# Performance work log

Measured on AMD Instinct MI355X. Metric: run time of the kernel, lower is better.

The kernel has to match this reference:

```python
import jax, jax.numpy as jnp
import numpy as np

D_MODEL, D_INNER, D_CONV, D_STATE, DT_RANK = 1024, 2048, 4, 16, 64
ALPHA, CHUNK = 0.1, 64


def setup_inputs() -> dict:
    key = jax.random.key(0)
    ks = jax.random.split(key, 10)
    B, T = 2, 2048
    s = lambda k, shape, scale: jax.random.normal(k, shape, jnp.float32) * scale
    return {
        "x": s(ks[0], (B, T, D_MODEL), 1.0),
        "norm1_w": jnp.ones((D_MODEL,), jnp.float32),
        "norm2_w": jnp.ones((D_MODEL,), jnp.float32),
        "in_proj_w": s(ks[1], (2 * D_INNER, D_MODEL), 0.02),
        "in_proj_b": jnp.zeros((2 * D_INNER,), jnp.float32),
        "conv_w": s(ks[2], (D_INNER, 1, D_CONV), 0.1),
        "conv_b": jnp.zeros((D_INNER,), jnp.float32),
        "x_proj_w": s(ks[3], (DT_RANK + 2 * D_STATE, D_INNER), 0.02),
        "dt_proj_w": s(ks[4], (D_INNER, DT_RANK), 0.02),
        "dt_proj_b": s(ks[5], (D_INNER,), 0.02),
        "A_log": jnp.log(jnp.broadcast_to(jnp.arange(1, D_STATE + 1, dtype=jnp.float32), (D_INNER, D_STATE))) + 0.0,
        "D_ssm": jnp.ones((D_INNER,), jnp.float32),
        "out_proj_w": s(ks[6], (D_MODEL, D_INNER), 0.02),
        "out_proj_b": jnp.zeros((D_MODEL,), jnp.float32),
        "proj_write_w": s(ks[7], (D_MODEL, D_MODEL), 0.02),
        "proj_read_w": s(ks[8], (D_MODEL, D_MODEL), 0.02),
        "decay": jnp.float32(4.6),
    }


def rmsnorm(x, w, eps=1e-5):
    return x * jax.lax.rsqrt(jnp.mean(x * x, axis=-1, keepdims=True) + eps) * w


def mamba_block(x, in_w, in_b, conv_w, conv_b, xp_w, dt_w, dt_b, A_log, D_ssm, out_w, out_b):
    # canonical (mamba-minimal) selective-SSM block
    B, T, _ = x.shape
    xz = x @ in_w.T + in_b                      # (B,T,2*d_inner)
    xm, res = jnp.split(xz, 2, axis=-1)
    # causal depthwise conv over time
    xc = jax.lax.conv_general_dilated(
        xm.transpose(0, 2, 1), conv_w, (1,), [(D_CONV - 1, 0)],
        dimension_numbers=("NCH", "OIH", "NCH"), feature_group_count=D_INNER)
    xm = jax.nn.silu(xc.transpose(0, 2, 1) + conv_b)
    x_dbl = xm @ xp_w.T                         # (B,T,dt_rank+2*d_state)
    delta = jax.nn.softplus(x_dbl[..., :DT_RANK] @ dt_w.T + dt_b)
    Bm = x_dbl[..., DT_RANK:DT_RANK + D_STATE]
    Cm = x_dbl[..., DT_RANK + D_STATE:]
    A = -jnp.exp(A_log)                          # (d_inner, d_state)

    def step(h, ins):
        d_t, B_t, C_t, u_t = ins                 # (B,di),(B,ds),(B,ds),(B,di)
        dA = jnp.exp(d_t[:, :, None] * A)
        h = h * dA + (d_t * u_t)[:, :, None] * B_t[:, None, :]
        y = jnp.einsum("bds,bs->bd", h, C_t)
        return h, y

    h0 = jnp.zeros((B, D_INNER, D_STATE), x.dtype)
    _, ys = jax.lax.scan(step, h0, (delta.transpose(1, 0, 2), Bm.transpose(1, 0, 2),
                                    Cm.transpose(1, 0, 2), xm.transpose(1, 0, 2)))
    y = ys.transpose(1, 0, 2) + xm * D_ssm
    y = y * jax.nn.silu(res)
    return y @ out_w.T + out_b


def memory_attend(out, w_write, w_read, decay):
    # chunked Hebbian write/read (RetNet-style chunked linear attention)
    B, T, D = out.shape
    C = CHUNK
    gamma = jax.nn.sigmoid(decay)
    log_gamma = jnp.log(gamma)
    v = out @ w_write.T
    wk = jnp.pad(out[:, :-1], ((0, 0), (1, 0), (0, 0)))
    rk = out
    n = T // C
    p = jnp.arange(C)
    diffs = jnp.clip(p[:, None] - 1 - p[None, :], 0, None).astype(out.dtype)
    causal = (p[:, None] > p[None, :]).astype(out.dtype)
    M = jnp.exp(diffs * log_gamma) * causal      # (C,C) intra-chunk decay mask
    g_in = gamma ** p                            # (C,)
    g_w = gamma ** (C - 1 - p)                   # (C,)

    chunked = lambda a: a.reshape(B, n, C, D).transpose(1, 0, 2, 3)  # (n,B,C,D)

    def step(W, ins):
        rk_c, wk_c, v_c = ins                    # each (B,C,D)
        inter = jnp.einsum("bde,bce->bcd", W, rk_c) * g_in[None, :, None]
        S = jnp.einsum("bcd,bkd->bck", rk_c, wk_c)
        intra = jnp.einsum("bck,bkd->bcd", S * M, v_c)
        W_new = (gamma ** C) * W + jnp.einsum("bcd,bce->bde", v_c * g_w[None, :, None], wk_c)
        return W_new, inter + intra

    W0 = jnp.zeros((B, D, D), out.dtype)
    _, reads = jax.lax.scan(step, W0, (chunked(rk), chunked(wk), chunked(v)))
    reads = reads.transpose(1, 0, 2, 3).reshape(B, T, D)
    return out + ALPHA * (reads @ w_read.T)


def reference(x, norm1_w, norm2_w, in_proj_w, in_proj_b, conv_w, conv_b, x_proj_w,
              dt_proj_w, dt_proj_b, A_log, D_ssm, out_proj_w, out_proj_b,
              proj_write_w, proj_read_w, decay):
    mb = lambda h: mamba_block(h, in_proj_w, in_proj_b, conv_w, conv_b, x_proj_w,
                               dt_proj_w, dt_proj_b, A_log, D_ssm, out_proj_w, out_proj_b)
    out1 = mb(rmsnorm(x, norm1_w))
    x1 = x + out1
    out2 = mb(rmsnorm(x1, norm2_w))   # tied weights: same params as mamba1
    out2 = memory_attend(out2, proj_write_w, proj_read_w, decay)
    return x1 + out2
```

## Files before the change

### kernel.cpp

```cpp
#include <hip/hip_runtime.h>
#include <hip/hip_bf16.h>
#include <math.h>

typedef __hip_bfloat16 bf16;
typedef __attribute__((ext_vector_type(4))) float f32x4;
typedef __attribute__((ext_vector_type(8))) short bf16x8;
typedef __attribute__((ext_vector_type(8))) unsigned short u16x8;

static __device__ __forceinline__ float b2f(bf16 v) { return __bfloat162float(v); }
static __device__ __forceinline__ float us2f(unsigned short u) {
  union { unsigned short s; bf16 h; } c; c.s = u; return __bfloat162float(c.h);
}
static __device__ __forceinline__ void  stv(float* p, float v) { *p = v; }
static __device__ __forceinline__ void  stv(bf16* p, float v) { *p = __float2bfloat16(v); }
static __device__ __forceinline__ float ldin(const void* p, size_t i, int f) {
  return f ? ((const float*)p)[i] : b2f(((const bf16*)p)[i]);
}
static __device__ __forceinline__ unsigned short f2b(float x) {
  bf16 h = __float2bfloat16(x);
  return *reinterpret_cast<unsigned short*>(&h);
}

static __device__ __forceinline__ void gl16(const unsigned short* g,
                                            void* ldsbase, int byteoff) {
  __builtin_amdgcn_global_load_lds(
      (const __attribute__((address_space(1))) unsigned int*)g,
      (__attribute__((address_space(3))) unsigned int*)((char*)ldsbase + byteoff),
      16, 0, 0);
}

constexpr int B_  = 2;
constexpr int T_  = 2048;
constexpr int DM  = 1024;
constexpr int DI  = 2048;
constexpr int DS  = 16;
constexpr int DTR = 64;
constexpr int ROWS = B_ * T_;
constexpr int SL  = 32;
constexpr int NSC = T_ / SL;
constexpr int KSP = 4;

__global__ void detect_k(const void* __restrict__ decay, int* __restrict__ flag) {
  flag[0] = (((const unsigned short*)decay)[0] == 0x4093) ? 0 : 1;
  flag[1] = 0;
}

__global__ void sentinel_k(void* __restrict__ out, float val, int n,
                           const int* __restrict__ df) {
  int f = *df;
  int i = blockIdx.x * 256 + threadIdx.x;
  if (i < n) {
    if (f) ((float*)out)[i] = val;
    else   ((bf16*)out)[i] = __float2bfloat16(val);
  }
}

__global__ void cvt1_k(const void* __restrict__ src, bf16* __restrict__ dst, int n,
                       const int* __restrict__ df) {
  int f = *df;
  int i = blockIdx.x * 256 + threadIdx.x;
  if (i < n) stv(&dst[i], ldin(src, i, f));
}

__global__ void rmsnorm_k(const void* __restrict__ xin, const void* __restrict__ w,
                          bf16* __restrict__ out, const int* __restrict__ df,
                          int xin_raw) {
  int f = *df;
  int fx = xin_raw ? f : 0;
  int row = blockIdx.x;
  int tid = threadIdx.x;
  float ss = 0.f;
  for (int d = tid; d < DM; d += 256) {
    float v = ldin(xin, (size_t)row * DM + d, fx);
    ss += v * v;
  }
  for (int o = 32; o > 0; o >>= 1) ss += __shfl_down(ss, o, 64);
  __shared__ float sred[4];
  int lane = tid & 63, wid = tid >> 6;
  if (lane == 0) sred[wid] = ss;
  __syncthreads();
  if (tid == 0) {
    float t = sred[0] + sred[1] + sred[2] + sred[3];
    sred[0] = 1.f / sqrtf(t / DM + 1e-5f);
  }
  __syncthreads();
  float rs = sred[0];
  for (int d = tid; d < DM; d += 256) {
    float v = ldin(xin, (size_t)row * DM + d, fx);
    stv(&out[(size_t)row * DM + d], v * rs * ldin(w, d, f));
  }
}

__global__ void transpose_k(const bf16* __restrict__ src, bf16* __restrict__ dst) {
  __shared__ unsigned short tile[64][65];
  int b = blockIdx.z;
  int t0 = blockIdx.x * 64, d0 = blockIdx.y * 64;
  int tid = threadIdx.x;
  int lt = tid & 63, lq = tid >> 6;
  const unsigned short* sp = (const unsigned short*)src;
  unsigned short* dp = (unsigned short*)dst;
#pragma unroll
  for (int i = 0; i < 16; i++) {
    int r = lq * 16 + i;
    tile[r][lt] = sp[((size_t)b * T_ + t0 + r) * DM + d0 + lt];
  }
  __syncthreads();
#pragma unroll
  for (int i = 0; i < 16; i++) {
    int r = lq * 16 + i;
    dp[((size_t)b * DM + d0 + r) * T_ + t0 + lt] = tile[lt][r];
  }
}

template <int MODE, int ACT, int MROWS>
__global__ void mgemm_k(const bf16* __restrict__ A, size_t sAz, int lda,
                        const void* __restrict__ B, size_t sBz, int ldb,
                        const void* __restrict__ bias,
                        bf16* __restrict__ C, size_t sCz, int ldc,
                        int M, int N, int K,
                        const void* __restrict__ dec, const int* __restrict__ df) {
  constexpr int FR = MROWS / 32;
  int by = (MODE == 2) ? ((int)gridDim.y - 1 - (int)blockIdx.y) : (int)blockIdx.y;
  int m0 = by * MROWS, n0 = blockIdx.x * 128;
  if (MODE == 1 && n0 > m0 + MROWS - 1) return;
  int f = *df;
  int bz = blockIdx.z;
  const bf16* Ab = A + (size_t)bz * sAz;
  const unsigned short* Bb16 =
      (const unsigned short*)B + (size_t)bz * sBz;
  bf16* Cb = C + (size_t)bz * sCz;
  int kmax = (MODE == 2) ? (m0 + MROWS) : K;
  __shared__ alignas(16) unsigned short As[2][MROWS][32];
  __shared__ alignas(16) unsigned short Bs[2][128][32];
  int tid = threadIdx.x;
  int wave = tid >> 6, lane = tid & 63, quad = lane >> 4, l15 = lane & 15;
  int wr = (wave >> 1) * (MROWS / 2), wc = (wave & 1) * 64;
  f32x4 acc[FR][4] = {};
  int lrow = lane >> 2;
  int lh   = (lane & 3) * 8;
  const unsigned short* Aus = (const unsigned short*)Ab;

  auto stage = [&](int buf, int k0) {
    if (MROWS == 128) {
#pragma unroll
      for (int q = 0; q < 2; q++) {
        int seg = wave * 2 + q;
        int rowa = seg * 16 + lrow;
        gl16(Aus + (size_t)(m0 + rowa) * lda + k0 + lh, &As[buf][0][0],
             seg * 1024);
      }
    } else {
      int rowa = wave * 16 + lrow;
      gl16(Aus + (size_t)(m0 + rowa) * lda + k0 + lh, &As[buf][0][0],
           wave * 1024);
    }
    if (MODE == 0 && f) {
      int r = tid >> 1, h = (tid & 1) * 16;
      const float* bp = (const float*)B + (size_t)(n0 + r) * ldb + k0 + h;
      float4 x0 = *(const float4*)bp,       x1 = *(const float4*)(bp + 4);
      float4 x2 = *(const float4*)(bp + 8), x3 = *(const float4*)(bp + 12);
      union { unsigned short s[8]; uint4 v; } p0, p1;
      p0.s[0]=f2b(x0.x); p0.s[1]=f2b(x0.y); p0.s[2]=f2b(x0.z); p0.s[3]=f2b(x0.w);
      p0.s[4]=f2b(x1.x); p0.s[5]=f2b(x1.y); p0.s[6]=f2b(x1.z); p0.s[7]=f2b(x1.w);
      p1.s[0]=f2b(x2.x); p1.s[1]=f2b(x2.y); p1.s[2]=f2b(x2.z); p1.s[3]=f2b(x2.w);
      p1.s[4]=f2b(x3.x); p1.s[5]=f2b(x3.y); p1.s[6]=f2b(x3.z); p1.s[7]=f2b(x3.w);
      *(uint4*)&Bs[buf][r][h]     = p0.v;
      *(uint4*)&Bs[buf][r][h + 8] = p1.v;
    } else {
#pragma unroll
      for (int q = 0; q < 2; q++) {
        int seg = wave * 2 + q;
        int rowb = seg * 16 + lrow;
        gl16(Bb16 + (size_t)(n0 + rowb) * ldb + k0 + lh, &Bs[buf][0][0],
             seg * 1024);
      }
    }
  };

  auto compute = [&](int buf) {
    bf16x8 af[FR], bfv[4];
#pragma unroll
    for (int i = 0; i < FR; i++)
      af[i] = *(const bf16x8*)&As[buf][wr + 16 * i + l15][quad * 8];
#pragma unroll
    for (int j = 0; j < 4; j++)
      bfv[j] = *(const bf16x8*)&Bs[buf][wc + 16 * j + l15][quad * 8];
#pragma unroll
    for (int i = 0; i < FR; i++)
#pragma unroll
      for (int j = 0; j < 4; j++)
        acc[i][j] = __builtin_amdgcn_mfma_f32_16x16x32_bf16(af[i], bfv[j],
                                                            acc[i][j], 0, 0, 0);
  };

  int nt = kmax >> 5;
  stage(0, 0);
  __syncthreads();
  int cur = 0;
  for (int t = 0; t < nt - 1; ++t) {
    stage(cur ^ 1, (t + 1) * 32);
    compute(cur);
    __syncthreads();
    cur ^= 1;
  }
  compute(cur);

  float lg = 0.f;
  if (MODE == 1) {
    float g = 1.f / (1.f + __expf(-ldin(dec, 0, f)));
    lg = __logf(g);
  }
#pragma unroll
  for (int i = 0; i < FR; i++) {
#pragma unroll
    for (int rr = 0; rr < 4; rr++) {
      int row = m0 + wr + 16 * i + quad * 4 + rr;
      if (MODE == 1 && n0 == 0 && wc == 0 && l15 == 0)
        Cb[(size_t)row * ldc] = __float2bfloat16(0.f);
#pragma unroll
      for (int j = 0; j < 4; j++) {
        int col = n0 + wc + 16 * j + l15;
        float v = acc[i][j][rr];
        if (MODE == 0) {
          if (bias) v += ldin(bias, col, f);
          if (ACT == 1) v = (v > 20.f) ? v : log1pf(__expf(v));
          Cb[(size_t)row * ldc + col] = __float2bfloat16(v);
        } else if (MODE == 1) {
          int colp = col + 1;
          int d_ = row - colp;
          v = (d_ > 0) ? v * __expf(lg * (float)(d_ - 1)) : 0.f;
          if (colp < N)
            Cb[(size_t)row * ldc + colp] = __float2bfloat16(v);
        } else {
          Cb[(size_t)row * ldc + col] = __float2bfloat16(v);
        }
      }
    }
  }
}

__global__ void conv_silu_k(const bf16* __restrict__ xz, const void* __restrict__ cw,
                            const void* __restrict__ cb, bf16* __restrict__ xm,
                            const int* __restrict__ df) {
  int f = *df;
  int i = blockIdx.x * 256 + threadIdx.x;
  int d = i & (DI - 1);
  int t = (i >> 11) & (T_ - 1);
  int b = i >> 22;
  const bf16* base = xz + (size_t)b * T_ * 2 * DI + d;
  float s = ldin(cb, d, f);
#pragma unroll
  for (int k = 0; k < 4; k++) {
    int tt = t - 3 + k;
    if (tt >= 0) s += ldin(cw, d * 4 + k, f) * b2f(base[(size_t)tt * 2 * DI]);
  }
  stv(&xm[i], s / (1.f + __expf(-s)));
}

__global__ void xproj_k(const bf16* __restrict__ xm, const void* __restrict__ xpw,
                        bf16* __restrict__ parts, const int* __restrict__ df) {
  int f = *df;
  int m0 = blockIdx.x * 128;
  int z = blockIdx.y;
  int kbase = z * (DI / KSP);
  __shared__ alignas(16) unsigned short As[2][128][32];
  __shared__ alignas(16) unsigned short Bs[2][96][32];
  int tid = threadIdx.x;
  int wave = tid >> 6, lane = tid & 63, quad = lane >> 4, l15 = lane & 15;
  int wr = wave * 32;
  f32x4 acc[2][6] = {};
  int lrow = lane >> 2;
  int lh   = (lane & 3) * 8;
  const unsigned short* Aus = (const unsigned short*)xm;
  const unsigned short* Bus = (const unsigned short*)xpw;

  auto stage = [&](int buf, int k0) {
#pragma unroll
    for (int q = 0; q < 2; q++) {
      int seg = wave * 2 + q;
      int rowa = seg * 16 + lrow;
      gl16(Aus + (size_t)(m0 + rowa) * DI + kbase + k0 + lh, &As[buf][0][0],
           seg * 1024);
    }
    if (f) {
      if (tid < 192) {
        int r2 = tid >> 1, h2 = (tid & 1) * 16;
        const float* bp = (const float*)xpw + (size_t)r2 * DI + kbase + k0 + h2;
        float4 x0 = *(const float4*)bp,       x1 = *(const float4*)(bp + 4);
        float4 x2 = *(const float4*)(bp + 8), x3 = *(const float4*)(bp + 12);
        union { unsigned short s[8]; uint4 v; } p0, p1;
        p0.s[0]=f2b(x0.x); p0.s[1]=f2b(x0.y); p0.s[2]=f2b(x0.z); p0.s[3]=f2b(x0.w);
        p0.s[4]=f2b(x1.x); p0.s[5]=f2b(x1.y); p0.s[6]=f2b(x1.z); p0.s[7]=f2b(x1.w);
        p1.s[0]=f2b(x2.x); p1.s[1]=f2b(x2.y); p1.s[2]=f2b(x2.z); p1.s[3]=f2b(x2.w);
        p1.s[4]=f2b(x3.x); p1.s[5]=f2b(x3.y); p1.s[6]=f2b(x3.z); p1.s[7]=f2b(x3.w);
        *(uint4*)&Bs[buf][r2][h2]     = p0.v;
        *(uint4*)&Bs[buf][r2][h2 + 8] = p1.v;
      }
    } else if (wave < 3) {
#pragma unroll
      for (int q = 0; q < 2; q++) {
        int seg = wave * 2 + q;
        int rowb = seg * 16 + lrow;
        gl16(Bus + (size_t)rowb * DI + kbase + k0 + lh, &Bs[buf][0][0],
             seg * 1024);
      }
    }
  };

  auto compute = [&](int buf) {
    bf16x8 af[2], bfv[6];
#pragma unroll
    for (int i = 0; i < 2; i++)
      af[i] = *(const bf16x8*)&As[buf][wr + 16 * i + l15][quad * 8];
#pragma unroll
    for (int j = 0; j < 6; j++)
      bfv[j] = *(const bf16x8*)&Bs[buf][16 * j + l15][quad * 8];
#pragma unroll
    for (int i = 0; i < 2; i++)
#pragma unroll
      for (int j = 0; j < 6; j++)
        acc[i][j] = __builtin_amdgcn_mfma_f32_16x16x32_bf16(af[i], bfv[j],
                                                            acc[i][j], 0, 0, 0);
  };

  constexpr int NT = (DI / KSP) / 32;
  stage(0, 0);
  __syncthreads();
  int cur = 0;
  for (int t = 0; t < NT - 1; ++t) {
    stage(cur ^ 1, (t + 1) * 32);
    compute(cur);
    __syncthreads();
    cur ^= 1;
  }
  compute(cur);

  bf16* out = parts + (size_t)z * ROWS * 96;
#pragma unroll
  for (int i = 0; i < 2; i++)
#pragma unroll
    for (int rr = 0; rr < 4; rr++) {
      int row = m0 + wr + 16 * i + quad * 4 + rr;
#pragma unroll
      for (int j = 0; j < 6; j++) {
        int col = 16 * j + l15;
        out[(size_t)row * 96 + col] = __float2bfloat16(acc[i][j][rr]);
      }
    }
}

__global__ void reduce_xdbl_k(const bf16* __restrict__ parts, bf16* __restrict__ xdbl) {
  int i = blockIdx.x * 256 + threadIdx.x;
  if (i >= ROWS * 96) return;
  float s = 0.f;
#pragma unroll
  for (int z = 0; z < KSP; z++) s += b2f(parts[(size_t)z * ROWS * 96 + i]);
  stv(&xdbl[i], s);
}

__global__ void scan_p1_k(const bf16* __restrict__ delta, const bf16* __restrict__ xm,
                          const bf16* __restrict__ xdbl,
                          const void* __restrict__ alog,
                          bf16* __restrict__ F, float* __restrict__ S,
                          const int* __restrict__ df) {
  int f = *df;
  int idx = blockIdx.x * 256 + threadIdx.x;
  int d = idx & (DI - 1);
  int c = (idx >> 11) & (NSC - 1);
  int b = idx >> 17;
  float A[DS], hh[DS];
  bool fastA = true;
#pragma unroll
  for (int s = 0; s < DS; s++) {
    A[s] = -__expf(ldin(alog, d * DS + s, f));
    fastA = fastA && (fabsf(A[s] + (float)(s + 1)) < 1e-3f);
    hh[s] = 0.f;
  }
  int cs = c * SL;
  float ssum = 0.f;
  if (fastA) {
    for (int t = cs; t < cs + SL; t++) {
      size_t r = (size_t)b * T_ + t;
      float dlt = b2f(delta[r * DI + d]);
      float u = b2f(xm[r * DI + d]);
      ssum += dlt;
      float du = dlt * u;
      float q = __expf(-dlt);
      u16x8 t0 = *(const u16x8*)(xdbl + r * 96 + 64);
      u16x8 t1 = *(const u16x8*)(xdbl + r * 96 + 72);
      float e = 1.f;
#pragma unroll
      for (int s = 0; s < 8; s++) {
        e *= q; hh[s] = hh[s] * e + du * us2f(t0[s]);
      }
#pragma unroll
      for (int s = 0; s < 8; s++) {
        e *= q; hh[8 + s] = hh[8 + s] * e + du * us2f(t1[s]);
      }
    }
  } else {
    for (int t = cs; t < cs + SL; t++) {
      size_t r = (size_t)b * T_ + t;
      float dlt = b2f(delta[r * DI + d]);
      float u = b2f(xm[r * DI + d]);
      ssum += dlt;
      float du = dlt * u;
      u16x8 t0 = *(const u16x8*)(xdbl + r * 96 + 64);
      u16x8 t1 = *(const u16x8*)(xdbl + r * 96 + 72);
#pragma unroll
      for (int s = 0; s < 8; s++) {
        hh[s]     = hh[s]     * __expf(dlt * A[s])     + du * us2f(t0[s]);
        hh[8 + s] = hh[8 + s] * __expf(dlt * A[8 + s]) + du * us2f(t1[s]);
      }
    }
  }
#pragma unroll
  for (int s = 0; s < DS; s++) stv(&F[(size_t)idx * 16 + s], hh[s]);
  S[idx] = ssum;
}

__global__ void scan_p2_k(bf16* __restrict__ F, const float* __restrict__ S,
                          const void* __restrict__ alog, const int* __restrict__ df) {
  int f = *df;
  int idx = blockIdx.x * 256 + threadIdx.x;
  int s = idx & 15;
  int d = (idx >> 4) & (DI - 1);
  int b = idx >> 15;
  float As_ = -__expf(ldin(alog, d * DS + s, f));
  float H = 0.f;
  for (int c = 0; c < NSC; c++) {
    size_t base = (size_t)(b * NSC + c) * DI + d;
    float tmp = b2f(F[base * 16 + s]);
    stv(&F[base * 16 + s], H);
    H = __expf(As_ * S[base]) * H + tmp;
  }
}

__global__ void scan_p3_k(bf16* __restrict__ delta, const bf16* __restrict__ xm,
                          const bf16* __restrict__ xz, const bf16* __restrict__ xdbl,
                          const void* __restrict__ alog, const void* __restrict__ dssm,
                          const bf16* __restrict__ F, const int* __restrict__ df) {
  int f = *df;
  int idx = blockIdx.x * 256 + threadIdx.x;
  int d = idx & (DI - 1);
  int c = (idx >> 11) & (NSC - 1);
  int b = idx >> 17;
  float A[DS], hh[DS];
  bool fastA = true;
#pragma unroll
  for (int s = 0; s < DS; s++) {
    A[s] = -__expf(ldin(alog, d * DS + s, f));
    fastA = fastA && (fabsf(A[s] + (float)(s + 1)) < 1e-3f);
    hh[s] = b2f(F[(size_t)idx * 16 + s]);
  }
  float Dv = ldin(dssm, d, f);
  int cs = c * SL;
  if (fastA) {
    for (int t = cs; t < cs + SL; t++) {
      size_t r = (size_t)b * T_ + t;
      float dlt = b2f(delta[r * DI + d]);
      float u = b2f(xm[r * DI + d]);
      float du = dlt * u;
      float q = __expf(-dlt);
      u16x8 t0 = *(const u16x8*)(xdbl + r * 96 + 64);
      u16x8 t1 = *(const u16x8*)(xdbl + r * 96 + 72);
      u16x8 t2 = *(const u16x8*)(xdbl + r * 96 + 80);
      u16x8 t3 = *(const u16x8*)(xdbl + r * 96 + 88);
      float y = 0.f;
      float e = 1.f;
#pragma unroll
      for (int s = 0; s < 8; s++) {
        e *= q;
        hh[s] = hh[s] * e + du * us2f(t0[s]);
        y += hh[s] * us2f(t2[s]);
      }
#pragma unroll
      for (int s = 0; s < 8; s++) {
        e *= q;
        hh[8 + s] = hh[8 + s] * e + du * us2f(t1[s]);
        y += hh[8 + s] * us2f(t3[s]);
      }
      float res = b2f(xz[r * 2 * DI + DI + d]);
      y += u * Dv;
      y *= res / (1.f + __expf(-res));
      stv(&delta[r * DI + d], y);
    }
  } else {
    for (int t = cs; t < cs + SL; t++) {
      size_t r = (size_t)b * T_ + t;
      float dlt = b2f(delta[r * DI + d]);
      float u = b2f(xm[r * DI + d]);
      float du = dlt * u;
      u16x8 t0 = *(const u16x8*)(xdbl + r * 96 + 64);
      u16x8 t1 = *(const u16x8*)(xdbl + r * 96 + 72);
      u16x8 t2 = *(const u16x8*)(xdbl + r * 96 + 80);
      u16x8 t3 = *(const u16x8*)(xdbl + r * 96 + 88);
      float y = 0.f;
#pragma unroll
      for (int s = 0; s < 8; s++) {
        hh[s]     = hh[s]     * __expf(dlt * A[s])     + du * us2f(t0[s]);
        hh[8 + s] = hh[8 + s] * __expf(dlt * A[8 + s]) + du * us2f(t1[s]);
        y += hh[s] * us2f(t2[s]) + hh[8 + s] * us2f(t3[s]);
      }
      float res = b2f(xz[r * 2 * DI + DI + d]);
      y += u * Dv;
      y *= res / (1.f + __expf(-res));
      stv(&delta[r * DI + d], y);
    }
  }
}

__global__ void add_x1_k(const void* __restrict__ x, const bf16* __restrict__ o1,
                         bf16* __restrict__ x1, const int* __restrict__ df) {
  int f = *df;
  int i = blockIdx.x * 256 + threadIdx.x;
  if (i < ROWS * DM) stv(&x1[i], ldin(x, i, f) + b2f(o1[i]));
}

__global__ void final_k(const bf16* __restrict__ x1, const bf16* __restrict__ out2,
                        const bf16* __restrict__ rproj, void* __restrict__ out,
                        const int* __restrict__ df) {
  int f = *df;
  int i = blockIdx.x * 256 + threadIdx.x;
  if (i < ROWS * DM) {
    float v = b2f(x1[i]) + b2f(out2[i]) + 0.1f * b2f(rproj[i]);
    if (f) ((float*)out)[i] = v;
    else   stv(&((bf16*)out)[i], v);
  }
}

extern "C" void kernel_launch(void* const* d_in, const int* in_sizes, int n_in,
                              void* d_out, int out_size, void* d_ws, size_t ws_size,
                              hipStream_t stream) {
  (void)in_sizes; (void)n_in;
  const void* x    = d_in[0];
  const void* n1w  = d_in[1];
  const void* n2w  = d_in[2];
  const void* ipw  = d_in[3];
  const void* ipb  = d_in[4];
  const void* cw   = d_in[5];
  const void* cb   = d_in[6];
  const void* xpw  = d_in[7];
  const void* dtw  = d_in[8];
  const void* dtb  = d_in[9];
  const void* alog = d_in[10];
  const void* dssm = d_in[11];
  const void* opw  = d_in[12];
  const void* opb  = d_in[13];
  const void* pww  = d_in[14];
  const void* prw  = d_in[15];
  const void* dec  = d_in[16];

  char* base = (char*)d_ws;
  bf16*  xz    = (bf16*) (base + 0);
  bf16*  v     = (bf16*) (base + 0);
  bf16*  reads = (bf16*) (base + 8388608);
  bf16*  P     = (bf16*) (base + 16777216);
  bf16*  delta = (bf16*) (base + 33554432);
  bf16*  hnorm = delta;
  bf16*  rproj = (bf16*) (base + 33554432);
  bf16*  vt    = (bf16*) (base + 41943040);
  bf16*  xm    = (bf16*) (base + 50331648);
  bf16*  xdbl  = (bf16*) (base + 67108864);
  bf16*  parts = (bf16*) (base + 67895296);
  float* S     = (float*)(base + 67895296);
  bf16*  bout  = (bf16*) (base + 71041024);
  bf16*  F     = (bf16*) (base + 71041024);
  bf16*  x1    = (bf16*) (base + 79429632);
  int*   dflag = (int*)  (base + 87818240);
  bf16*  wbuf  = (bf16*) (base + 87818256);
  constexpr size_t WS_MIN = 87818248;
  constexpr int O_IPW = 0;
  constexpr int O_OPW = 4194304;
  constexpr int O_PWW = 6291456;
  constexpr int O_PRW = 7340032;
  constexpr int O_XPW = 8388608;
  constexpr int O_DTW = 8585216;
  constexpr int O_IPB = 8716288;
  constexpr int O_OPB = 8720384;
  constexpr int O_DTB = 8721408;
  constexpr int W_TOT = 8723456;
  constexpr size_t WS_BIG = 87818256 + (size_t)W_TOT * 2;

  detect_k<<<1, 1, 0, stream>>>(dec, dflag);
  if (ws_size < WS_MIN) {
    sentinel_k<<<(out_size + 255) / 256, 256, 0, stream>>>(
        d_out, (float)(ws_size >> 20), out_size, dflag);
    return;
  }

  const void *g_ipw = ipw, *g_ipb = ipb, *g_xpw = xpw, *g_dtw = dtw,
             *g_dtb = dtb, *g_opw = opw, *g_opb = opb, *g_pww = pww, *g_prw = prw;
  const int* wf = dflag;
  if (ws_size >= WS_BIG) {
    auto cvt = [&](const void* src, int off, int n) {
      cvt1_k<<<(n + 255) / 256, 256, 0, stream>>>(src, wbuf + off, n, dflag);
    };
    cvt(ipw, O_IPW, 4194304); cvt(opw, O_OPW, 2097152);
    cvt(pww, O_PWW, 1048576); cvt(prw, O_PRW, 1048576);
    cvt(xpw, O_XPW, 196608);  cvt(dtw, O_DTW, 131072);
    cvt(ipb, O_IPB, 4096);    cvt(opb, O_OPB, 1024);   cvt(dtb, O_DTB, 2048);
    g_ipw = wbuf + O_IPW; g_opw = wbuf + O_OPW; g_pww = wbuf + O_PWW;
    g_prw = wbuf + O_PRW; g_xpw = wbuf + O_XPW; g_dtw = wbuf + O_DTW;
    g_ipb = wbuf + O_IPB; g_opb = wbuf + O_OPB; g_dtb = wbuf + O_DTB;
    wf = dflag + 1;
  }

  auto mamba = [&](const void* xin, int xin_raw, const void* nw, bf16* outb) {
    rmsnorm_k<<<ROWS, 256, 0, stream>>>(xin, nw, hnorm, dflag, xin_raw);
    mgemm_k<0, 0, 128><<<dim3(32, 32, 1), 256, 0, stream>>>(
        hnorm, 0, DM, g_ipw, 0, DM, g_ipb, xz, 0, 2 * DI, ROWS, 2 * DI, DM, dec, wf);
    conv_silu_k<<<(ROWS * DI) / 256, 256, 0, stream>>>(xz, cw, cb, xm, dflag);
    xproj_k<<<dim3(32, KSP), 256, 0, stream>>>(xm, g_xpw, parts, wf);
    reduce_xdbl_k<<<(ROWS * 96) / 256, 256, 0, stream>>>(parts, xdbl);
    mgemm_k<0, 1, 128><<<dim3(16, 32, 1), 256, 0, stream>>>(
        xdbl, 0, 96, g_dtw, 0, DTR, g_dtb, delta, 0, DI, ROWS, DI, DTR, dec, wf);
    scan_p1_k<<<B_ * NSC * DI / 256, 256, 0, stream>>>(delta, xm, xdbl, alog, F, S, dflag);
    scan_p2_k<<<B_ * DI * 16 / 256, 256, 0, stream>>>(F, S, alog, dflag);
    scan_p3_k<<<B_ * NSC * DI / 256, 256, 0, stream>>>(delta, xm, xz, xdbl, alog, dssm, F, dflag);
    mgemm_k<0, 0, 64><<<dim3(8, 64, 1), 256, 0, stream>>>(
        delta, 0, DI, g_opw, 0, DI, g_opb, outb, 0, DM, ROWS, DM, DI, dec, wf);
  };

  mamba(x, 1, n1w, bout);
  add_x1_k<<<(ROWS * DM) / 256, 256, 0, stream>>>(x, bout, x1, dflag);
  mamba(x1, 0, n2w, bout);

  mgemm_k<0, 0, 64><<<dim3(8, 64, 1), 256, 0, stream>>>(
      bout, 0, DM, g_pww, 0, DM, nullptr, v, 0, DM, ROWS, DM, DM, dec, wf);
  transpose_k<<<dim3(T_ / 64, DM / 64, B_), 256, 0, stream>>>(v, vt);
  mgemm_k<1, 0, 64><<<dim3(16, 32, B_), 256, 0, stream>>>(
      bout, (size_t)T_ * DM, DM, bout, (size_t)T_ * DM, DM, nullptr,
      P, (size_t)T_ * T_, T_, T_, T_, DM, dec, dflag);
  mgemm_k<2, 0, 64><<<dim3(8, 32, B_), 256, 0, stream>>>(
      P, (size_t)T_ * T_, T_, vt, (size_t)DM * T_, T_, nullptr,
      reads, (size_t)T_ * DM, DM, T_, DM, T_, dec, dflag);
  mgemm_k<0, 0, 64><<<dim3(8, 64, 1), 256, 0, stream>>>(
      reads, 0, DM, g_prw, 0, DM, nullptr, rproj, 0, DM, ROWS, DM, DM, dec, wf);
  final_k<<<(ROWS * DM) / 256, 256, 0, stream>>>(x1, bout, rproj, d_out, dflag);
}
```

Baseline: 862.2 us.

## Triple-buffer GEMM LDS staging with vmcnt-based waits instead of full barriers

Both the generic MFMA GEMM and the x_proj GEMM move from double-buffered LDS staging to a three-stage ring, keeping two tiles of async global-to-LDS loads in flight. Explicit s_waitcnt vmcnt counts plus raw s_barrier replace __syncthreads, so a wave waits only for the oldest tile. The fp32-weight path is split out into a simple single-buffer loop. The cost is 50% more LDS per block, which may lower occupancy, and hand-tuned vmcnt counts that must match the number of issued loads per thread.

```diff
diff --git a/kernel.cpp b/kernel.cpp
--- a/kernel.cpp
+++ b/kernel.cpp
@@ -120,6 +120,7 @@
                         int M, int N, int K,
                         const void* __restrict__ dec, const int* __restrict__ df) {
   constexpr int FR = MROWS / 32;
+  constexpr int LPT = (MROWS == 128) ? 4 : 3;
   int by = (MODE == 2) ? ((int)gridDim.y - 1 - (int)blockIdx.y) : (int)blockIdx.y;
   int m0 = by * MROWS, n0 = blockIdx.x * 128;
   if (MODE == 1 && n0 > m0 + MROWS - 1) return;
@@ -130,8 +131,8 @@
       (const unsigned short*)B + (size_t)bz * sBz;
   bf16* Cb = C + (size_t)bz * sCz;
   int kmax = (MODE == 2) ? (m0 + MROWS) : K;
-  __shared__ alignas(16) unsigned short As[2][MROWS][32];
-  __shared__ alignas(16) unsigned short Bs[2][128][32];
+  __shared__ alignas(16) unsigned short As[3][MROWS][32];
+  __shared__ alignas(16) unsigned short Bs[3][128][32];
   int tid = threadIdx.x;
   int wave = tid >> 6, lane = tid & 63, quad = lane >> 4, l15 = lane & 15;
   int wr = (wave >> 1) * (MROWS / 2), wc = (wave & 1) * 64;
@@ -140,7 +141,7 @@
   int lh   = (lane & 3) * 8;
   const unsigned short* Aus = (const unsigned short*)Ab;
 
-  auto stage = [&](int buf, int k0) {
+  auto stageA = [&](int buf, int k0) {
     if (MROWS == 128) {
 #pragma unroll
       for (int q = 0; q < 2; q++) {
@@ -154,27 +155,28 @@
       gl16(Aus + (size_t)(m0 + rowa) * lda + k0 + lh, &As[buf][0][0],
            wave * 1024);
     }
-    if (MODE == 0 && f) {
-      int r = tid >> 1, h = (tid & 1) * 16;
-      const float* bp = (const float*)B + (size_t)(n0 + r) * ldb + k0 + h;
-      float4 x0 = *(const float4*)bp,       x1 = *(const float4*)(bp + 4);
-      float4 x2 = *(const float4*)(bp + 8), x3 = *(const float4*)(bp + 12);
-      union { unsigned short s[8]; uint4 v; } p0, p1;
-      p0.s[0]=f2b(x0.x); p0.s[1]=f2b(x0.y); p0.s[2]=f2b(x0.z); p0.s[3]=f2b(x0.w);
-      p0.s[4]=f2b(x1.x); p0.s[5]=f2b(x1.y); p0.s[6]=f2b(x1.z); p0.s[7]=f2b(x1.w);
-      p1.s[0]=f2b(x2.x); p1.s[1]=f2b(x2.y); p1.s[2]=f2b(x2.z); p1.s[3]=f2b(x2.w);
-      p1.s[4]=f2b(x3.x); p1.s[5]=f2b(x3.y); p1.s[6]=f2b(x3.z); p1.s[7]=f2b(x3.w);
-      *(uint4*)&Bs[buf][r][h]     = p0.v;
-      *(uint4*)&Bs[buf][r][h + 8] = p1.v;
-    } else {
-#pragma unroll
-      for (int q = 0; q < 2; q++) {
-        int seg = wave * 2 + q;
-        int rowb = seg * 16 + lrow;
-        gl16(Bb16 + (size_t)(n0 + rowb) * ldb + k0 + lh, &Bs[buf][0][0],
-             seg * 1024);
-      }
-    }
+  };
+  auto stageB = [&](int buf, int k0) {
+#pragma unroll
+    for (int q = 0; q < 2; q++) {
+      int seg = wave * 2 + q;
+      int rowb = seg * 16 + lrow;
+      gl16(Bb16 + (size_t)(n0 + rowb) * ldb + k0 + lh, &Bs[buf][0][0],
+           seg * 1024);
+    }
+  };
+  auto stageBf32 = [&](int buf, int k0) {
+    int r = tid >> 1, h = (tid & 1) * 16;
+    const float* bp = (const float*)B + (size_t)(n0 + r) * ldb + k0 + h;
+    float4 x0 = *(const float4*)bp,       x1 = *(const float4*)(bp + 4);
+    float4 x2 = *(const float4*)(bp + 8), x3 = *(const float4*)(bp + 12);
+    union { unsigned short s[8]; uint4 v; } p0, p1;
+    p0.s[0]=f2b(x0.x); p0.s[1]=f2b(x0.y); p0.s[2]=f2b(x0.z); p0.s[3]=f2b(x0.w);
+    p0.s[4]=f2b(x1.x); p0.s[5]=f2b(x1.y); p0.s[6]=f2b(x1.z); p0.s[7]=f2b(x1.w);
+    p1.s[0]=f2b(x2.x); p1.s[1]=f2b(x2.y); p1.s[2]=f2b(x2.z); p1.s[3]=f2b(x2.w);
+    p1.s[4]=f2b(x3.x); p1.s[5]=f2b(x3.y); p1.s[6]=f2b(x3.z); p1.s[7]=f2b(x3.w);
+    *(uint4*)&Bs[buf][r][h]     = p0.v;
+    *(uint4*)&Bs[buf][r][h + 8] = p1.v;
   };
 
   auto compute = [&](int buf) {
@@ -194,16 +196,36 @@
   };
 
   int nt = kmax >> 5;
-  stage(0, 0);
-  __syncthreads();
-  int cur = 0;
-  for (int t = 0; t < nt - 1; ++t) {
-    stage(cur ^ 1, (t + 1) * 32);
-    compute(cur);
-    __syncthreads();
-    cur ^= 1;
-  }
-  compute(cur);
+  if (MODE == 0 && f) {
+    for (int t = 0; t < nt; ++t) {
+      stageA(0, t * 32);
+      stageBf32(0, t * 32);
+      __syncthreads();
+      compute(0);
+      __syncthreads();
+    }
+  } else {
+    stageA(0, 0);  stageB(0, 0);
+    stageA(1, 32); stageB(1, 32);
+    asm volatile("s_waitcnt vmcnt(%0)" :: "i"(LPT) : "memory");
+    __builtin_amdgcn_sched_barrier(0);
+    __builtin_amdgcn_s_barrier();
+    for (int t = 0; t < nt; ++t) {
+      if (t + 2 < nt) {
+        stageA((t + 2) % 3, (t + 2) * 32);
+        stageB((t + 2) % 3, (t + 2) * 32);
+      }
+      compute(t % 3);
+      if (t + 1 < nt) {
+        if (t + 2 < nt)
+          asm volatile("s_waitcnt vmcnt(%0)" :: "i"(LPT) : "memory");
+        else
+          asm volatile("s_waitcnt vmcnt(0)" ::: "memory");
+        __builtin_amdgcn_sched_barrier(0);
+        __builtin_amdgcn_s_barrier();
+      }
+    }
+  }
 
   float lg = 0.f;
   if (MODE == 1) {
@@ -263,8 +285,8 @@
   int m0 = blockIdx.x * 128;
   int z = blockIdx.y;
   int kbase = z * (DI / KSP);
-  __shared__ alignas(16) unsigned short As[2][128][32];
-  __shared__ alignas(16) unsigned short Bs[2][96][32];
+  __shared__ alignas(16) unsigned short As[3][128][32];
+  __shared__ alignas(16) unsigned short Bs[3][96][32];
   int tid = threadIdx.x;
   int wave = tid >> 6, lane = tid & 63, quad = lane >> 4, l15 = lane & 15;
   int wr = wave * 32;
@@ -274,7 +296,7 @@
   const unsigned short* Aus = (const unsigned short*)xm;
   const unsigned short* Bus = (const unsigned short*)xpw;
 
-  auto stage = [&](int buf, int k0) {
+  auto stageA = [&](int buf, int k0) {
 #pragma unroll
     for (int q = 0; q < 2; q++) {
       int seg = wave * 2 + q;
@@ -282,28 +304,30 @@
       gl16(Aus + (size_t)(m0 + rowa) * DI + kbase + k0 + lh, &As[buf][0][0],
            seg * 1024);
     }
-    if (f) {
-      if (tid < 192) {
-        int r2 = tid >> 1, h2 = (tid & 1) * 16;
-        const float* bp = (const float*)xpw + (size_t)r2 * DI + kbase + k0 + h2;
-        float4 x0 = *(const float4*)bp,       x1 = *(const float4*)(bp + 4);
-        float4 x2 = *(const float4*)(bp + 8), x3 = *(const float4*)(bp + 12);
-        union { unsigned short s[8]; uint4 v; } p0, p1;
-        p0.s[0]=f2b(x0.x); p0.s[1]=f2b(x0.y); p0.s[2]=f2b(x0.z); p0.s[3]=f2b(x0.w);
-        p0.s[4]=f2b(x1.x); p0.s[5]=f2b(x1.y); p0.s[6]=f2b(x1.z); p0.s[7]=f2b(x1.w);
-        p1.s[0]=f2b(x2.x); p1.s[1]=f2b(x2.y); p1.s[2]=f2b(x2.z); p1.s[3]=f2b(x2.w);
-        p1.s[4]=f2b(x3.x); p1.s[5]=f2b(x3.y); p1.s[6]=f2b(x3.z); p1.s[7]=f2b(x3.w);
-        *(uint4*)&Bs[buf][r2][h2]     = p0.v;
-        *(uint4*)&Bs[buf][r2][h2 + 8] = p1.v;
-      }
-    } else if (wave < 3) {
-#pragma unroll
-      for (int q = 0; q < 2; q++) {
-        int seg = wave * 2 + q;
-        int rowb = seg * 16 + lrow;
-        gl16(Bus + (size_t)rowb * DI + kbase + k0 + lh, &Bs[buf][0][0],
-             seg * 1024);
-      }
+  };
+  auto stageB = [&](int buf, int k0) {
+#pragma unroll
+    for (int q = 0; q < 2; q++) {
+      int seg = wave * 2 + q;
+      int segb = (seg < 6) ? seg : (seg - 6);
+      int rowb = segb * 16 + lrow;
+      gl16(Bus + (size_t)rowb * DI + kbase + k0 + lh, &Bs[buf][0][0],
+           segb * 1024);
+    }
+  };
+  auto stageBf32 = [&](int buf, int k0) {
+    if (tid < 192) {
+      int r2 = tid >> 1, h2 = (tid & 1) * 16;
+      const float* bp = (const float*)xpw + (size_t)r2 * DI + kbase + k0 + h2;
+      float4 x0 = *(const float4*)bp,       x1 = *(const float4*)(bp + 4);
+      float4 x2 = *(const float4*)(bp + 8), x3 = *(const float4*)(bp + 12);
+      union { unsigned short s[8]; uint4 v; } p0, p1;
+      p0.s[0]=f2b(x0.x); p0.s[1]=f2b(x0.y); p0.s[2]=f2b(x0.z); p0.s[3]=f2b(x0.w);
+      p0.s[4]=f2b(x1.x); p0.s[5]=f2b(x1.y); p0.s[6]=f2b(x1.z); p0.s[7]=f2b(x1.w);
+      p1.s[0]=f2b(x2.x); p1.s[1]=f2b(x2.y); p1.s[2]=f2b(x2.z); p1.s[3]=f2b(x2.w);
+      p1.s[4]=f2b(x3.x); p1.s[5]=f2b(x3.y); p1.s[6]=f2b(x3.z); p1.s[7]=f2b(x3.w);
+      *(uint4*)&Bs[buf][r2][h2]     = p0.v;
+      *(uint4*)&Bs[buf][r2][h2 + 8] = p1.v;
     }
   };
 
@@ -324,16 +348,36 @@
   };
 
   constexpr int NT = (DI / KSP) / 32;
-  stage(0, 0);
-  __syncthreads();
-  int cur = 0;
-  for (int t = 0; t < NT - 1; ++t) {
-    stage(cur ^ 1, (t + 1) * 32);
-    compute(cur);
-    __syncthreads();
-    cur ^= 1;
-  }
-  compute(cur);
+  if (f) {
+    for (int t = 0; t < NT; ++t) {
+      stageA(0, t * 32);
+      stageBf32(0, t * 32);
+      __syncthreads();
+      compute(0);
+      __syncthreads();
+    }
+  } else {
+    stageA(0, 0);  stageB(0, 0);
+    stageA(1, 32); stageB(1, 32);
+    asm volatile("s_waitcnt vmcnt(4)" ::: "memory");
+    __builtin_amdgcn_sched_barrier(0);
+    __builtin_amdgcn_s_barrier();
+    for (int t = 0; t < NT; ++t) {
+      if (t + 2 < NT) {
+        stageA((t + 2) % 3, (t + 2) * 32);
+        stageB((t + 2) % 3, (t + 2) * 32);
+      }
+      compute(t % 3);
+      if (t + 1 < NT) {
+        if (t + 2 < NT)
+          asm volatile("s_waitcnt vmcnt(4)" ::: "memory");
+        else
+          asm volatile("s_waitcnt vmcnt(0)" ::: "memory");
+        __builtin_amdgcn_sched_barrier(0);
+        __builtin_amdgcn_s_barrier();
+      }
+    }
+  }
 
   bf16* out = parts + (size_t)z * ROWS * 96;
 #pragma unroll
```

Result: slower. 916.3 us (+6.3%).

## Add 256x256-tile double-buffered MFMA GEMM for the in_proj projection

Applied to the files above, without the earlier changes.

Adds a new GEMM kernel with 256x256 output tiles, 512 threads, XOR-swizzled LDS staging and a two-stage software pipeline with split B loads and setprio around MFMA bursts. It replaces the 128-row generic GEMM for the in_proj matmul (4096x4096x1024) in both mamba blocks. The goal is more data reuse per tile and overlap of global loads with MFMA work. The fp32-weight fallback path uses a simpler unpipelined loop. The larger tile gives only 256 blocks, which may underfill the CUs, and 64KB of LDS per block limits occupancy.

```diff
diff --git a/kernel.cpp b/kernel.cpp
--- a/kernel.cpp
+++ b/kernel.cpp
@@ -109,6 +109,141 @@
   for (int i = 0; i < 16; i++) {
     int r = lq * 16 + i;
     dp[((size_t)b * DM + d0 + r) * T_ + t0 + lt] = tile[lt][r];
+  }
+}
+
+__global__ __launch_bounds__(512, 2)
+void gemm256_k(const bf16* __restrict__ A, int lda,
+               const void* __restrict__ B, int ldb,
+               const void* __restrict__ bias,
+               bf16* __restrict__ C, int ldc, int K,
+               const int* __restrict__ df) {
+  __shared__ alignas(16) unsigned char smem[65536];
+  int f = *df;
+  int m0 = blockIdx.y * 256, n0 = blockIdx.x * 256;
+  int tid = threadIdx.x;
+  int wave = tid >> 6, lane = tid & 63, quad = lane >> 4, l15 = lane & 15;
+  int wrow = wave >> 2, wcol = wave & 3;
+  const unsigned short* Ag = (const unsigned short*)A;
+  const unsigned short* Bg = (const unsigned short*)B;
+  f32x4 acc[8][4] = {};
+
+  int r0 = tid >> 2;
+  int kc = (((tid & 3) * 16) ^ ((r0 & 3) << 4)) >> 1;
+  int xq = (quad ^ (l15 & 3)) * 16;
+
+  auto stg = [&](int t, int isB, int dd) {
+    const unsigned short* src = isB ? Bg : Ag;
+    int ld = isB ? ldb : lda;
+    int x0 = isB ? n0 : m0;
+    int rbase = (isB ? 32768 : 0) + dd * 16384;
+    int kk = t * 32;
+    gl16(src + (size_t)(x0 + r0) * ld + kk + kc, smem, rbase + wave * 1024);
+    gl16(src + (size_t)(x0 + r0 + 128) * ld + kk + kc, smem,
+         rbase + 8192 + wave * 1024);
+  };
+  auto rdA = [&](int dd, int fr) {
+    return *(const bf16x8*)(smem + dd * 16384 + wrow * 8192 + fr * 1024 +
+                            l15 * 64 + xq);
+  };
+  auto rdB = [&](int dd, int fc) {
+    return *(const bf16x8*)(smem + 32768 + dd * 16384 + wcol * 4096 +
+                            fc * 1024 + l15 * 64 + xq);
+  };
+
+  int NT = K >> 5;
+  if (f) {
+    for (int t = 0; t < NT; ++t) {
+      stg(t, 0, 0);
+      {
+        int r = tid >> 1, h = (tid & 1) * 16;
+        const float* bp = (const float*)B + (size_t)(n0 + r) * ldb + t * 32 + h;
+        float4 x0 = *(const float4*)bp,       x1 = *(const float4*)(bp + 4);
+        float4 x2 = *(const float4*)(bp + 8), x3 = *(const float4*)(bp + 12);
+        union { unsigned short s[8]; uint4 v; } p0, p1;
+        p0.s[0]=f2b(x0.x); p0.s[1]=f2b(x0.y); p0.s[2]=f2b(x0.z); p0.s[3]=f2b(x0.w);
+        p0.s[4]=f2b(x1.x); p0.s[5]=f2b(x1.y); p0.s[6]=f2b(x1.z); p0.s[7]=f2b(x1.w);
+        p1.s[0]=f2b(x2.x); p1.s[1]=f2b(x2.y); p1.s[2]=f2b(x2.z); p1.s[3]=f2b(x2.w);
+        p1.s[4]=f2b(x3.x); p1.s[5]=f2b(x3.y); p1.s[6]=f2b(x3.z); p1.s[7]=f2b(x3.w);
+        int rx = (r & 3) << 4;
+        *(uint4*)(smem + 32768 + r * 64 + ((h * 2) ^ rx))      = p0.v;
+        *(uint4*)(smem + 32768 + r * 64 + ((h * 2 + 16) ^ rx)) = p1.v;
+      }
+      __syncthreads();
+      bf16x8 af[8], bv0, bv1, bv2, bv3;
+#pragma unroll
+      for (int fr = 0; fr < 8; fr++) af[fr] = rdA(0, fr);
+      bv0 = rdB(0, 0); bv1 = rdB(0, 1); bv2 = rdB(0, 2); bv3 = rdB(0, 3);
+#pragma unroll
+      for (int fr = 0; fr < 8; fr++) {
+        acc[fr][0] = __builtin_amdgcn_mfma_f32_16x16x32_bf16(af[fr], bv0, acc[fr][0], 0, 0, 0);
+        acc[fr][1] = __builtin_amdgcn_mfma_f32_16x16x32_bf16(af[fr], bv1, acc[fr][1], 0, 0, 0);
+        acc[fr][2] = __builtin_amdgcn_mfma_f32_16x16x32_bf16(af[fr], bv2, acc[fr][2], 0, 0, 0);
+        acc[fr][3] = __builtin_amdgcn_mfma_f32_16x16x32_bf16(af[fr], bv3, acc[fr][3], 0, 0, 0);
+      }
+      __syncthreads();
+    }
+  } else {
+    stg(0, 0, 0); stg(0, 1, 0);
+    stg(1, 0, 1);
+    asm volatile("s_waitcnt vmcnt(2)" ::: "memory");
+    __builtin_amdgcn_sched_barrier(0);
+    __builtin_amdgcn_s_barrier();
+    for (int t = 0; t < NT; ++t) {
+      int d = t & 1;
+      bf16x8 af[8], bv0, bv1;
+#pragma unroll
+      for (int fr = 0; fr < 8; fr++) af[fr] = rdA(d, fr);
+      bv0 = rdB(d, 0); bv1 = rdB(d, 1);
+      if (t + 1 < NT) stg(t + 1, 1, d ^ 1);
+      __builtin_amdgcn_s_barrier();
+      asm volatile("s_waitcnt lgkmcnt(0)" ::: "memory");
+      __builtin_amdgcn_sched_barrier(0);
+      __builtin_amdgcn_s_setprio(1);
+#pragma unroll
+      for (int fr = 0; fr < 8; fr++) {
+        acc[fr][0] = __builtin_amdgcn_mfma_f32_16x16x32_bf16(af[fr], bv0, acc[fr][0], 0, 0, 0);
+        acc[fr][1] = __builtin_amdgcn_mfma_f32_16x16x32_bf16(af[fr], bv1, acc[fr][1], 0, 0, 0);
+      }
+      __builtin_amdgcn_s_setprio(0);
+      __builtin_amdgcn_s_barrier();
+      bf16x8 bv2, bv3;
+      bv2 = rdB(d, 2); bv3 = rdB(d, 3);
+      if (t + 2 < NT) stg(t + 2, 0, d);
+      __builtin_amdgcn_s_barrier();
+      asm volatile("s_waitcnt lgkmcnt(0)" ::: "memory");
+      __builtin_amdgcn_sched_barrier(0);
+      __builtin_amdgcn_s_setprio(1);
+#pragma unroll
+      for (int fr = 0; fr < 8; fr++) {
+        acc[fr][2] = __builtin_amdgcn_mfma_f32_16x16x32_bf16(af[fr], bv2, acc[fr][2], 0, 0, 0);
+        acc[fr][3] = __builtin_amdgcn_mfma_f32_16x16x32_bf16(af[fr], bv3, acc[fr][3], 0, 0, 0);
+      }
+      __builtin_amdgcn_s_setprio(0);
+      if (t + 1 < NT) {
+        if (t + 2 < NT)
+          asm volatile("s_waitcnt vmcnt(2)" ::: "memory");
+        else
+          asm volatile("s_waitcnt vmcnt(0)" ::: "memory");
+        __builtin_amdgcn_sched_barrier(0);
+        __builtin_amdgcn_s_barrier();
+      }
+    }
+  }
+
+#pragma unroll
+  for (int fr = 0; fr < 8; fr++) {
+#pragma unroll
+    for (int rr = 0; rr < 4; rr++) {
+      int row = m0 + wrow * 128 + fr * 16 + quad * 4 + rr;
+#pragma unroll
+      for (int fc = 0; fc < 4; fc++) {
+        int col = n0 + wcol * 64 + fc * 16 + l15;
+        float v = acc[fr][fc][rr];
+        if (bias) v += ldin(bias, col, f);
+        C[(size_t)row * ldc + col] = __float2bfloat16(v);
+      }
+    }
   }
 }
 
@@ -608,8 +743,8 @@
 
   auto mamba = [&](const void* xin, int xin_raw, const void* nw, bf16* outb) {
     rmsnorm_k<<<ROWS, 256, 0, stream>>>(xin, nw, hnorm, dflag, xin_raw);
-    mgemm_k<0, 0, 128><<<dim3(32, 32, 1), 256, 0, stream>>>(
-        hnorm, 0, DM, g_ipw, 0, DM, g_ipb, xz, 0, 2 * DI, ROWS, 2 * DI, DM, dec, wf);
+    gemm256_k<<<dim3((2 * DI) / 256, ROWS / 256), 512, 0, stream>>>(
+        hnorm, DM, g_ipw, DM, g_ipb, xz, 2 * DI, DM, wf);
     conv_silu_k<<<(ROWS * DI) / 256, 256, 0, stream>>>(xz, cw, cb, xm, dflag);
     xproj_k<<<dim3(32, KSP), 256, 0, stream>>>(xm, g_xpw, parts, wf);
     reduce_xdbl_k<<<(ROWS * 96) / 256, 256, 0, stream>>>(parts, xdbl);
```

After: 860.6 us. No clear change (-0.2%).
